# Performance work log

Hardware: AMD Instinct MI355X
Metric: run time of the kernel (lower is better)

## Reference

```python
import jax, jax.numpy as jnp
import numpy as np

EPS = 1e-6


def layernorm(x, w, b):
    m = jnp.mean(x, axis=-1, keepdims=True)
    v = jnp.var(x, axis=-1, keepdims=True)
    return (x - m) * jax.lax.rsqrt(v + EPS) * w + b


def rotate_half(x):
    x1, x2 = jnp.split(x, 2, axis=-1)
    return jnp.concatenate((-x2, x1), axis=-1)


def setup_inputs() -> dict:
    key = jax.random.key(0)
    ks = jax.random.split(key, 16)
    T, D, H, HD, I = 16384, 1280, 16, 80, 5120
    NSEG = 16
    inp = {
        "hidden_states": jax.random.normal(ks[0], (T, D), jnp.float32),
        "cos": jax.random.uniform(ks[1], (T, HD), jnp.float32),
        "sin": jax.random.uniform(ks[2], (T, HD), jnp.float32),
        "ln1_w": jnp.ones((D,), jnp.float32),
        "ln1_b": jnp.zeros((D,), jnp.float32),
        "ln2_w": jnp.ones((D,), jnp.float32),
        "ln2_b": jnp.zeros((D,), jnp.float32),
        "qkv_w": jax.random.normal(ks[3], (3 * D, D), jnp.float32) * 0.02,
        "qkv_b": jnp.zeros((3 * D,), jnp.float32),
        "proj_w": jax.random.normal(ks[4], (D, D), jnp.float32) * 0.02,
        "proj_b": jnp.zeros((D,), jnp.float32),
        "fc1_w": jax.random.normal(ks[5], (I, D), jnp.float32) * 0.02,
        "fc1_b": jnp.zeros((I,), jnp.float32),
        "fc2_w": jax.random.normal(ks[6], (D, I), jnp.float32) * 0.02,
        "fc2_b": jnp.zeros((D,), jnp.float32),
        "cu_seqlens": jnp.arange(NSEG + 1, dtype=jnp.int32) * (T // NSEG),
    }
    return inp


def reference(hidden_states, cos, sin, ln1_w, ln1_b, ln2_w, ln2_b,
              qkv_w, qkv_b, proj_w, proj_b, fc1_w, fc1_b, fc2_w, fc2_b,
              cu_seqlens):
    T, D = hidden_states.shape
    H = 16
    HD = D // H
    nseg = cu_seqlens.shape[0] - 1  # equal-length segments by construction
    L = T // nseg

    x = layernorm(hidden_states, ln1_w, ln1_b)
    qkv = (x @ qkv_w.T + qkv_b).reshape(T, 3, H, HD)
    q, k, v = qkv[:, 0], qkv[:, 1], qkv[:, 2]  # [T, H, HD]

    # RoPE in fp32, cos/sin broadcast over heads
    c = cos[:, None, :]
    s = sin[:, None, :]
    q = q * c + rotate_half(q) * s
    k = k * c + rotate_half(k) * s

    # block-diagonal varlen attention: reshape into [nseg, L, H, HD]
    qs = q.reshape(nseg, L, H, HD)
    ks = k.reshape(nseg, L, H, HD)
    vs = v.reshape(nseg, L, H, HD)
    scale = 1.0 / jnp.sqrt(jnp.asarray(HD, jnp.float32))
    scores = jnp.einsum('slhd,smhd->shlm', qs, ks) * scale
    probs = jax.nn.softmax(scores, axis=-1)
    attn = jnp.einsum('shlm,smhd->slhd', probs, vs).reshape(T, D)

    attn_out = attn @ proj_w.T + proj_b
    h = hidden_states + attn_out

    y = layernorm(h, ln2_w, ln2_b)
    mlp = (jax.nn.silu(y @ fc1_w.T + fc1_b)) @ fc2_w.T + fc2_b
    return h + mlp
```

## Files before the change

### kernel.cpp

```cpp
#include <hip/hip_runtime.h>
#include <hip/hip_bf16.h>
#include <hip/hip_fp16.h>

typedef _Float16 f16;
typedef _Float16 f16x2 __attribute__((ext_vector_type(2)));
typedef _Float16 f16x4 __attribute__((ext_vector_type(4)));
typedef _Float16 f16x8 __attribute__((ext_vector_type(8)));
typedef float f32x4 __attribute__((ext_vector_type(4)));
typedef float f32x16 __attribute__((ext_vector_type(16)));
typedef int i32x4 __attribute__((ext_vector_type(4)));

#define T_TOK 16384
#define D_MOD 1280
#define N_QKV 3840
#define I_MLP 5120
#define N_HEAD 16
#define HD 80
#define SEG_L 1024

__device__ __forceinline__ void async16(const void* g, void* l) {
    __builtin_amdgcn_global_load_lds(
        (const __attribute__((address_space(1))) void*)g,
        (__attribute__((address_space(3))) void*)l, 16, 0, 0);
}

#define BAR()        asm volatile("s_barrier" ::: "memory")
#define WAIT_LGKM0() do { asm volatile("s_waitcnt lgkmcnt(0)" ::: "memory"); \
                          __builtin_amdgcn_sched_barrier(0); } while (0)
#define WAIT_VM(n)   asm volatile("s_waitcnt vmcnt(" #n ")" ::: "memory")

__device__ __forceinline__ int f2i(f16x2 v) { int r; __builtin_memcpy(&r, &v, 4); return r; }
__device__ __forceinline__ f16x2 i2f(int v) { f16x2 r; __builtin_memcpy(&r, &v, 4); return r; }

__global__ __launch_bounds__(256) void cast_f32_f16(
    const float* __restrict__ src, f16* __restrict__ dst, int n) {
    int i = blockIdx.x * 256 + threadIdx.x;
    if (i < n) dst[i] = (f16)src[i];
}

template <typename TIN>
__global__ __launch_bounds__(256) void ln_kernel(
    const TIN* __restrict__ x, const float* __restrict__ w,
    const float* __restrict__ b, f16* __restrict__ out) {
    const int t = blockIdx.x;
    const TIN* row = x + (size_t)t * D_MOD;
    float vals[5];
    float s = 0.f, s2 = 0.f;
    for (int i = 0; i < 5; ++i) {
        float v = (float)row[threadIdx.x + i * 256];
        vals[i] = v; s += v; s2 += v * v;
    }
    for (int off = 32; off > 0; off >>= 1) {
        s  += __shfl_down(s, off);
        s2 += __shfl_down(s2, off);
    }
    __shared__ float rs[4], rs2[4];
    int wv = threadIdx.x >> 6;
    if ((threadIdx.x & 63) == 0) { rs[wv] = s; rs2[wv] = s2; }
    __syncthreads();
    s  = rs[0] + rs[1] + rs[2] + rs[3];
    s2 = rs2[0] + rs2[1] + rs2[2] + rs2[3];
    float m = s * (1.f / D_MOD);
    float var = s2 * (1.f / D_MOD) - m * m;
    float rstd = rsqrtf(var + 1e-6f);
    for (int i = 0; i < 5; ++i) {
        int c = threadIdx.x + i * 256;
        out[(size_t)t * D_MOD + c] = (f16)((vals[i] - m) * rstd * w[c] + b[c]);
    }
}

__global__ __launch_bounds__(256) void rope_inplace(
    f16* __restrict__ q, f16* __restrict__ k,
    const float* __restrict__ cosb, const float* __restrict__ sinb) {
    int i = blockIdx.x * 256 + threadIdx.x;
    if (i >= T_TOK * N_HEAD * 40) return;
    int d = i % 40;
    int th = i / 40;
    int h = th & 15;
    int t = th >> 4;
    size_t i0 = ((size_t)h * T_TOK + t) * HD + d;
    size_t i1 = i0 + 40;
    float c0 = cosb[t * HD + d],      s0 = sinb[t * HD + d];
    float c1 = cosb[t * HD + d + 40], s1 = sinb[t * HD + d + 40];
    {
        float x0 = (float)q[i0], x1 = (float)q[i1];
        q[i0] = (f16)(x0 * c0 - x1 * s0);
        q[i1] = (f16)(x1 * c1 + x0 * s1);
    }
    {
        float x0 = (float)k[i0], x1 = (float)k[i1];
        k[i0] = (f16)(x0 * c0 - x1 * s0);
        k[i1] = (f16)(x1 * c1 + x0 * s1);
    }
}

#define EPI_QKV   0
#define EPI_PROJ  1
#define EPI_SILU  2
#define EPI_FC2A  3
#define EPI_FC2B  4

#define READ_A(MH) \
    _Pragma("unroll") for (int mi = 0; mi < 4; ++mi) { \
        const f16* pa = &LB[lb][MH][(wr * 64 + mi * 16 + lane16) * 64]; \
        aF[mi][0] = *(const f16x8*)&pa[ch0]; \
        aF[mi][1] = *(const f16x8*)&pa[ch1]; \
    }
#define READ_B(NH) \
    _Pragma("unroll") for (int ni = 0; ni < 2; ++ni) { \
        const f16* pb = &LB[lb][2 + NH][(wc * 32 + ni * 16 + lane16) * 64]; \
        bF[ni][0] = *(const f16x8*)&pb[ch0]; \
        bF[ni][1] = *(const f16x8*)&pb[ch1]; \
    }
#define DO_MFMA(MH, NH) \
    __builtin_amdgcn_s_setprio(1); \
    _Pragma("unroll") for (int mi = 0; mi < 4; ++mi) \
    _Pragma("unroll") for (int ni = 0; ni < 2; ++ni) { \
        acc[MH][NH][mi][ni] = __builtin_amdgcn_mfma_f32_16x16x32_f16( \
            aF[mi][0], bF[ni][0], acc[MH][NH][mi][ni], 0, 0, 0); \
        acc[MH][NH][mi][ni] = __builtin_amdgcn_mfma_f32_16x16x32_f16( \
            aF[mi][1], bF[ni][1], acc[MH][NH][mi][ni], 0, 0, 0); \
    } \
    __builtin_amdgcn_s_setprio(0);

template <int EPI>
__global__ __launch_bounds__(512, 2) void gemm_bt(
    const f16* __restrict__ A, const f16* __restrict__ B,
    const float* __restrict__ bias, const void* __restrict__ resid,
    void* __restrict__ out0, f16* __restrict__ out1, f16* __restrict__ out2,
    int M, int N, int K, int lda, int ldb, int ldo) {
    __shared__ __align__(16) f16 LB[2][4][8192];
    const int tid = threadIdx.x;
    const int w = tid >> 6;
    const int l = tid & 63;
    const int lane16 = l & 15, quad = l >> 4;
    const int wr = w >> 2, wc = w & 3;

    const int nx = gridDim.x;
    int id = blockIdx.y * nx + blockIdx.x;
    const int nwg = nx * gridDim.y;
    int tile = ((nwg & 7) == 0) ? ((id & 7) * (nwg >> 3) + (id >> 3)) : id;
    const int m0 = (tile / nx) * 256;
    const int n0 = (tile % nx) * 256;
    const int NT = K >> 6;

    const int rr = tid >> 3;
    const int cc = (tid & 7) ^ (rr & 7);
    const size_t ga_off = (size_t)rr * lda + cc * 8;
    const size_t gb_off = (size_t)rr * ldb + cc * 8;
    const int lds_off = w * 512;
    const int swz = lane16 & 7;
    const int ch0 = ((0 * 4 + quad) ^ swz) * 8;
    const int ch1 = ((1 * 4 + quad) ^ swz) * 8;

    f32x4 acc[2][2][4][2];
#pragma unroll
    for (int a = 0; a < 2; ++a)
#pragma unroll
        for (int b2 = 0; b2 < 2; ++b2)
#pragma unroll
            for (int c = 0; c < 4; ++c)
#pragma unroll
                for (int d = 0; d < 2; ++d)
                    acc[a][b2][c][d] = (f32x4){0.f, 0.f, 0.f, 0.f};

    const f16* Abase = A + (size_t)m0 * lda;
    const f16* Bbase = B + (size_t)n0 * ldb;
    auto stageA = [&](int buf, int ph, int t) {
        const f16* g = Abase + (size_t)(ph * 128) * lda + (size_t)t * 64 + ga_off;
        f16* lr = &LB[buf][ph][0] + lds_off;
        async16(g, lr);
        async16(g + (size_t)64 * lda, lr + 4096);
    };
    auto stageB = [&](int buf, int ph, int t) {
        const f16* g = Bbase + (size_t)(ph * 128) * ldb + (size_t)t * 64 + gb_off;
        f16* lr = &LB[buf][2 + ph][0] + lds_off;
        async16(g, lr);
        async16(g + (size_t)64 * ldb, lr + 4096);
    };

    stageA(0, 0, 0); stageB(0, 1, 0); stageA(0, 1, 0); stageB(0, 0, 0);
    if (NT > 1) {
        stageA(1, 0, 1); stageB(1, 1, 1); stageA(1, 1, 1);
        WAIT_VM(6);
    } else {
        WAIT_VM(0);
    }
    BAR();

    for (int t = 0; t < NT; ++t) {
        const int lb = t & 1;
        f16x8 aF[4][2], bF[2][2];
        READ_A(0); READ_B(0);
        { int tau = t + 1; if (tau < NT) stageB(tau & 1, 0, tau); }
        BAR(); WAIT_LGKM0();
        DO_MFMA(0, 0);
        BAR();
        READ_B(1);
        { int tau = t + 2; if (tau < NT) stageA(tau & 1, 0, tau); }
        BAR(); WAIT_LGKM0();
        DO_MFMA(0, 1);
        BAR();
        READ_A(1);
        { int tau = t + 2; if (tau < NT) stageB(tau & 1, 1, tau); }
        BAR(); WAIT_LGKM0();
        DO_MFMA(1, 1);
        BAR();
        READ_B(0);
        { int tau = t + 2; if (tau < NT) stageA(tau & 1, 1, tau); }
        BAR(); WAIT_LGKM0();
        DO_MFMA(1, 0);
        if (t < NT - 2) { WAIT_VM(6); } else { WAIT_VM(0); }
        BAR();
    }

#pragma unroll
    for (int mh = 0; mh < 2; ++mh)
#pragma unroll
    for (int mi = 0; mi < 4; ++mi) {
        const int row = m0 + mh * 128 + wr * 64 + mi * 16 + quad * 4;
#pragma unroll
        for (int nh = 0; nh < 2; ++nh)
#pragma unroll
        for (int ni = 0; ni < 2; ++ni) {
            const int col = n0 + nh * 128 + wc * 32 + ni * 16 + lane16;
            const f32x4 v4 = acc[mh][nh][mi][ni];
            float bv = (EPI == EPI_FC2B) ? 0.f : bias[col];
            if (EPI == EPI_QKV) {
                int g = col / D_MOD;
                int rem = col - g * D_MOD;
                int h = rem / HD, d = rem - h * HD;
                if (g == 2) {
                    f16x4 pk;
#pragma unroll
                    for (int r2 = 0; r2 < 4; ++r2) pk[r2] = (f16)(v4[r2] + bv);
                    f16* dst = out2 + ((size_t)h * HD + d) * T_TOK + row;
                    *(f16x4*)dst = pk;
                } else {
                    f16* dst = (g == 0) ? (f16*)out0 : out1;
                    size_t base = ((size_t)h * T_TOK) * HD + d;
#pragma unroll
                    for (int r2 = 0; r2 < 4; ++r2) {
                        float v = v4[r2] + bv;
                        dst[base + (size_t)(row + r2) * HD] = (f16)v;
                    }
                }
            } else {
#pragma unroll
                for (int r2 = 0; r2 < 4; ++r2) {
                    float v = v4[r2] + bv;
                    size_t idx = (size_t)(row + r2) * ldo + col;
                    if (EPI == EPI_PROJ) {
                        ((f16*)out0)[idx] = (f16)(v + ((const float*)resid)[idx]);
                    } else if (EPI == EPI_SILU) {
                        ((f16*)out0)[idx] = (f16)(v / (1.f + __expf(-v)));
                    } else if (EPI == EPI_FC2A) {
                        ((float*)out0)[idx] = v + (float)((const f16*)resid)[idx];
                    } else {
                        ((float*)out0)[idx] += v;
                    }
                }
            }
        }
    }
}

#undef READ_A
#undef READ_B
#undef DO_MFMA

__global__ __launch_bounds__(256, 2) void attn_kernel(
    const f16* __restrict__ q, const f16* __restrict__ k,
    const f16* __restrict__ vt, f16* __restrict__ out) {
    const int bid0 = blockIdx.x;
    const int bid = (bid0 & 7) * 256 + (bid0 >> 3);
    const int s = bid >> 7, h = (bid >> 3) & 15, qt = bid & 7;
    const int t0 = s * SEG_L;
    const int tid = threadIdx.x;
    const int w = tid >> 6, l = tid & 63;
    const int l31 = l & 31, hi = l >> 5;

    __shared__ __align__(16) f16 lK[64 * 128];
    __shared__ __align__(16) f16 lVt[96 * 64];
    __shared__ float lInv[128];

    const f16 scale = (f16)0.16132167f;

    const int qrow_g = t0 + qt * 128 + w * 32 + l31;
    const f16* qp = q + ((size_t)h * T_TOK + qrow_g) * HD;
    f16x8 qf[5];
#pragma unroll
    for (int ks = 0; ks < 5; ++ks) {
        f16x8 v = *(const f16x8*)&qp[(ks * 2 + hi) * 8];
        qf[ks] = v * scale;
    }

    const f16* kbase  = k  + (size_t)h * T_TOK * HD + (size_t)t0 * HD;
    const f16* vtbase = vt + (size_t)h * HD * T_TOK + t0;

    if (tid < 128) {
        int r = 80 + (tid >> 3), c = tid & 7;
        *(f16x8*)&lVt[r * 64 + ((c ^ (r & 7)) * 8)] = (f16x8){0,0,0,0,0,0,0,0};
    }

    f16x8 kreg[3], vreg[3];
    auto ld_tile = [&](int kt) {
#pragma unroll
        for (int j = 0; j < 3; ++j) {
            int idx = tid + j * 256;
            if (idx < 640) {
                int r = idx / 10, c = idx - r * 10;
                kreg[j] = *(const f16x8*)&kbase[(size_t)(kt * 64 + r) * HD + c * 8];
                int rv = idx >> 3, cv = idx & 7;
                vreg[j] = *(const f16x8*)&vtbase[(size_t)rv * T_TOK + kt * 64 + cv * 8];
            }
        }
    };
    auto st_tile = [&]() {
#pragma unroll
        for (int j = 0; j < 3; ++j) {
            int idx = tid + j * 256;
            if (idx < 640) {
                int r = idx / 10, c = idx - r * 10;
                *(f16x8*)&lK[r * 128 + ((c ^ (r & 7)) * 8)] = kreg[j];
                int rv = idx >> 3, cv = idx & 7;
                *(f16x8*)&lVt[rv * 64 + ((cv ^ (rv & 7)) * 8)] = vreg[j];
            }
        }
    };

    float lrow = 0.f;
    f32x16 zz;
#pragma unroll
    for (int i = 0; i < 16; ++i) zz[i] = 0.f;
    f32x16 oacc[3];
    oacc[0] = zz; oacc[1] = zz; oacc[2] = zz;

    ld_tile(0);
    st_tile();
    __syncthreads();

    for (int kt = 0; kt < 16; ++kt) {
        if (kt < 15) ld_tile(kt + 1);

#pragma unroll
        for (int ct = 0; ct < 2; ++ct) {
            f32x16 sc = zz;
#pragma unroll
            for (int ks = 0; ks < 5; ++ks) {
                const int row = ct * 32 + l31;
                f16x8 kf = *(const f16x8*)&lK[row * 128 +
                              (((ks * 2 + hi) ^ (l31 & 7)) * 8)];
                sc = __builtin_amdgcn_mfma_f32_32x32x16_f16(kf, qf[ks], sc, 0, 0, 0);
            }
            float pf[16];
#pragma unroll
            for (int r = 0; r < 16; ++r) {
                float p = __builtin_exp2f(fminf(sc[r], 14.f));
                lrow += p;
                pf[r] = p;
            }
            f16x2 own[4][2];
            int prt[4][2];
#pragma unroll
            for (int d = 0; d < 4; ++d) {
                own[d][0] = (f16x2){(f16)pf[4 * d + 0], (f16)pf[4 * d + 1]};
                own[d][1] = (f16x2){(f16)pf[4 * d + 2], (f16)pf[4 * d + 3]};
                prt[d][0] = __shfl_xor(f2i(own[d][0]), 32);
                prt[d][1] = __shfl_xor(f2i(own[d][1]), 32);
            }
#pragma unroll
            for (int kk2 = 0; kk2 < 2; ++kk2) {
                const int De = 2 * kk2, Do = 2 * kk2 + 1;
                i32x4 av;
                av[0] = hi ? prt[Do][0] : f2i(own[De][0]);
                av[1] = hi ? prt[Do][1] : f2i(own[De][1]);
                av[2] = hi ? f2i(own[Do][0]) : prt[De][0];
                av[3] = hi ? f2i(own[Do][1]) : prt[De][1];
                f16x8 af;
                __builtin_memcpy(&af, &av, 16);
                const int kkg = ct * 2 + kk2;
#pragma unroll
                for (int nt = 0; nt < 3; ++nt) {
                    const int vrow = nt * 32 + l31;
                    f16x8 vf = *(const f16x8*)&lVt[vrow * 64 +
                                  (((kkg * 2 + hi) ^ (l31 & 7)) * 8)];
                    oacc[nt] = __builtin_amdgcn_mfma_f32_32x32x16_f16(
                        af, vf, oacc[nt], 0, 0, 0);
                }
            }
        }
        __syncthreads();
        if (kt < 15) st_tile();
        __syncthreads();
    }

    lrow += __shfl_xor(lrow, 32);
    float inv = 1.f / lrow;
    lInv[w * 32 + l31] = inv;

    f16* obase = out + (size_t)(t0 + qt * 128 + w * 32) * D_MOD + h * HD;
#pragma unroll
    for (int nt = 0; nt < 3; ++nt) {
        const int hd = nt * 32 + l31;
        if (nt < 2 || l31 < 16) {
#pragma unroll
            for (int r = 0; r < 16; ++r) {
                const int qrow = (r & 3) + 8 * (r >> 2) + 4 * hi;
                obase[(size_t)qrow * D_MOD + hd] =
                    (f16)(oacc[nt][r] * lInv[w * 32 + qrow]);
            }
        }
    }
}

extern "C" void kernel_launch(void* const* d_in, const int* in_sizes, int n_in,
                              void* d_out, int out_size, void* d_ws, size_t ws_size,
                              hipStream_t stream) {
    const float* hidden = (const float*)d_in[0];
    const float* cosb   = (const float*)d_in[1];
    const float* sinb   = (const float*)d_in[2];
    const float* ln1w   = (const float*)d_in[3];
    const float* ln1b   = (const float*)d_in[4];
    const float* ln2w   = (const float*)d_in[5];
    const float* ln2b   = (const float*)d_in[6];
    const float* qkvw   = (const float*)d_in[7];
    const float* qkvb   = (const float*)d_in[8];
    const float* projw  = (const float*)d_in[9];
    const float* projb  = (const float*)d_in[10];
    const float* fc1w   = (const float*)d_in[11];
    const float* fc1b   = (const float*)d_in[12];
    const float* fc2w   = (const float*)d_in[13];
    const float* fc2b   = (const float*)d_in[14];
    float* out = (float*)d_out;

    f16* wqkv  = (f16*)d_ws;
    f16* wproj = wqkv  + 4915200;
    f16* wfc1  = wproj + 1638400;
    f16* wfc2  = wfc1  + 6553600;
    f16* qf    = wfc2  + 6553600;
    f16* kf    = qf    + 20971520;
    f16* vf    = kf    + 20971520;
    f16* xf    = vf    + 20971520;
    f16* hbuf  = xf    + 20971520;
    f16* attnf  = xf;
    f16* yf     = qf;
    f16* fc1out = kf;

    cast_f32_f16<<<(4915200 + 255) / 256, 256, 0, stream>>>(qkvw, wqkv, 4915200);
    cast_f32_f16<<<(1638400 + 255) / 256, 256, 0, stream>>>(projw, wproj, 1638400);
    cast_f32_f16<<<(6553600 + 255) / 256, 256, 0, stream>>>(fc1w, wfc1, 6553600);
    cast_f32_f16<<<(6553600 + 255) / 256, 256, 0, stream>>>(fc2w, wfc2, 6553600);

    ln_kernel<float><<<T_TOK, 256, 0, stream>>>(hidden, ln1w, ln1b, xf);

    gemm_bt<EPI_QKV><<<dim3(N_QKV / 256, T_TOK / 256), 512, 0, stream>>>(
        xf, wqkv, qkvb, nullptr, qf, kf, vf,
        T_TOK, N_QKV, D_MOD, D_MOD, D_MOD, 0);

    rope_inplace<<<(T_TOK * N_HEAD * 40) / 256, 256, 0, stream>>>(qf, kf, cosb, sinb);

    attn_kernel<<<2048, 256, 0, stream>>>(qf, kf, vf, attnf);

    gemm_bt<EPI_PROJ><<<dim3(D_MOD / 256, T_TOK / 256), 512, 0, stream>>>(
        attnf, wproj, projb, hidden, hbuf, nullptr, nullptr,
        T_TOK, D_MOD, D_MOD, D_MOD, D_MOD, D_MOD);

    ln_kernel<f16><<<T_TOK, 256, 0, stream>>>(hbuf, ln2w, ln2b, yf);

    for (int c = 0; c < 2; ++c) {
        gemm_bt<EPI_SILU><<<dim3(2560 / 256, T_TOK / 256), 512, 0, stream>>>(
            yf, wfc1 + (size_t)c * 2560 * D_MOD, fc1b + c * 2560, nullptr,
            fc1out, nullptr, nullptr,
            T_TOK, 2560, D_MOD, D_MOD, D_MOD, 2560);
        if (c == 0) {
            gemm_bt<EPI_FC2A><<<dim3(D_MOD / 256, T_TOK / 256), 512, 0, stream>>>(
                fc1out, wfc2, fc2b, hbuf, out, nullptr, nullptr,
                T_TOK, D_MOD, 2560, 2560, I_MLP, D_MOD);
        } else {
            gemm_bt<EPI_FC2B><<<dim3(D_MOD / 256, T_TOK / 256), 512, 0, stream>>>(
                fc1out, wfc2 + 2560, fc2b, nullptr, out, nullptr, nullptr,
                T_TOK, D_MOD, 2560, 2560, I_MLP, D_MOD);
        }
    }
}
```

Before: 1.393 ms.

## Restructure GEMM main loop with register double-buffered fragments and overlapped LDS reads

The GEMM inner loop is rescheduled so LDS fragment reads for the next phase are issued before the current phase's MFMAs, using two register sets for A and B fragments. Each phase now needs one barrier plus LDS wait instead of two barriers. The prologue loads both stages up front, and the A fragments for the next tile are prefetched at the end of each iteration. The aim is to hide LDS latency behind MFMA work and cut synchronization, at the cost of more VGPRs, which could hurt occupancy or cause spills under launch_bounds(512,2).

```diff
diff --git a/kernel.cpp b/kernel.cpp
--- a/kernel.cpp
+++ b/kernel.cpp
@@ -28,9 +28,9 @@
 #define WAIT_LGKM0() do { asm volatile("s_waitcnt lgkmcnt(0)" ::: "memory"); \
                           __builtin_amdgcn_sched_barrier(0); } while (0)
 #define WAIT_VM(n)   asm volatile("s_waitcnt vmcnt(" #n ")" ::: "memory")
+#define SCHED0()     __builtin_amdgcn_sched_barrier(0)
 
 __device__ __forceinline__ int f2i(f16x2 v) { int r; __builtin_memcpy(&r, &v, 4); return r; }
-__device__ __forceinline__ f16x2 i2f(int v) { f16x2 r; __builtin_memcpy(&r, &v, 4); return r; }
 
 __global__ __launch_bounds__(256) void cast_f32_f16(
     const float* __restrict__ src, f16* __restrict__ dst, int n) {
@@ -100,27 +100,25 @@
 #define EPI_FC2A  3
 #define EPI_FC2B  4
 
-#define READ_A(MH) \
+#define RD_A(DST, MH, BUF) \
     _Pragma("unroll") for (int mi = 0; mi < 4; ++mi) { \
-        const f16* pa = &LB[lb][MH][(wr * 64 + mi * 16 + lane16) * 64]; \
-        aF[mi][0] = *(const f16x8*)&pa[ch0]; \
-        aF[mi][1] = *(const f16x8*)&pa[ch1]; \
-    }
-#define READ_B(NH) \
+        const f16* pa = &LB[BUF][MH][(wr * 64 + mi * 16 + lane16) * 64]; \
+        DST[mi][0] = *(const f16x8*)&pa[ch0]; \
+        DST[mi][1] = *(const f16x8*)&pa[ch1]; \
+    }
+#define RD_B(DST, NH, BUF) \
     _Pragma("unroll") for (int ni = 0; ni < 2; ++ni) { \
-        const f16* pb = &LB[lb][2 + NH][(wc * 32 + ni * 16 + lane16) * 64]; \
-        bF[ni][0] = *(const f16x8*)&pb[ch0]; \
-        bF[ni][1] = *(const f16x8*)&pb[ch1]; \
-    }
-#define DO_MFMA(MH, NH) \
+        const f16* pb = &LB[BUF][2 + NH][(wc * 32 + ni * 16 + lane16) * 64]; \
+        DST[ni][0] = *(const f16x8*)&pb[ch0]; \
+        DST[ni][1] = *(const f16x8*)&pb[ch1]; \
+    }
+#define MFMA_PH(MH, NH, AARR, BARR) \
     __builtin_amdgcn_s_setprio(1); \
+    _Pragma("unroll") for (int h2 = 0; h2 < 2; ++h2) \
     _Pragma("unroll") for (int mi = 0; mi < 4; ++mi) \
-    _Pragma("unroll") for (int ni = 0; ni < 2; ++ni) { \
+    _Pragma("unroll") for (int ni = 0; ni < 2; ++ni) \
         acc[MH][NH][mi][ni] = __builtin_amdgcn_mfma_f32_16x16x32_f16( \
-            aF[mi][0], bF[ni][0], acc[MH][NH][mi][ni], 0, 0, 0); \
-        acc[MH][NH][mi][ni] = __builtin_amdgcn_mfma_f32_16x16x32_f16( \
-            aF[mi][1], bF[ni][1], acc[MH][NH][mi][ni], 0, 0, 0); \
-    } \
+            AARR[mi][h2], BARR[ni][h2], acc[MH][NH][mi][ni], 0, 0, 0); \
     __builtin_amdgcn_s_setprio(0);
 
 template <int EPI>
@@ -179,39 +177,39 @@
         async16(g + (size_t)64 * ldb, lr + 4096);
     };
 
-    stageA(0, 0, 0); stageB(0, 1, 0); stageA(0, 1, 0); stageB(0, 0, 0);
-    if (NT > 1) {
-        stageA(1, 0, 1); stageB(1, 1, 1); stageA(1, 1, 1);
-        WAIT_VM(6);
-    } else {
-        WAIT_VM(0);
-    }
+    f16x8 aF0[4][2], aF1[4][2], bF0[2][2], bF1[2][2];
+
+    stageA(0, 0, 0); stageB(0, 0, 0); stageB(0, 1, 0); stageA(0, 1, 0);
+    if (NT > 1) { stageA(1, 0, 1); stageB(1, 0, 1); stageB(1, 1, 1); stageA(1, 1, 1); }
+    WAIT_VM(0);
+    BAR();
+    RD_A(aF0, 0, 0);
+    WAIT_LGKM0();
     BAR();
 
     for (int t = 0; t < NT; ++t) {
         const int lb = t & 1;
-        f16x8 aF[4][2], bF[2][2];
-        READ_A(0); READ_B(0);
-        { int tau = t + 1; if (tau < NT) stageB(tau & 1, 0, tau); }
-        BAR(); WAIT_LGKM0();
-        DO_MFMA(0, 0);
-        BAR();
-        READ_B(1);
-        { int tau = t + 2; if (tau < NT) stageA(tau & 1, 0, tau); }
-        BAR(); WAIT_LGKM0();
-        DO_MFMA(0, 1);
-        BAR();
-        READ_A(1);
-        { int tau = t + 2; if (tau < NT) stageB(tau & 1, 1, tau); }
-        BAR(); WAIT_LGKM0();
-        DO_MFMA(1, 1);
-        BAR();
-        READ_B(0);
-        { int tau = t + 2; if (tau < NT) stageA(tau & 1, 1, tau); }
-        BAR(); WAIT_LGKM0();
-        DO_MFMA(1, 0);
+        RD_B(bF0, 0, lb);
+        RD_B(bF1, 1, lb);
+        if (t + 2 < NT) stageA(lb, 0, t + 2);
+        SCHED0();
+        MFMA_PH(0, 0, aF0, bF0);
+        WAIT_LGKM0(); BAR();
+        RD_A(aF1, 1, lb);
+        if (t + 2 < NT) stageB(lb, 1, t + 2);
+        SCHED0();
+        MFMA_PH(0, 1, aF0, bF1);
+        WAIT_LGKM0(); BAR();
+        if (t + 2 < NT) stageA(lb, 1, t + 2);
         if (t < NT - 2) { WAIT_VM(6); } else { WAIT_VM(0); }
-        BAR();
+        SCHED0();
+        MFMA_PH(1, 1, aF1, bF1);
+        WAIT_LGKM0(); BAR();
+        if (t + 2 < NT) stageB(lb, 0, t + 2);
+        if (t + 1 < NT) RD_A(aF0, 0, lb ^ 1);
+        SCHED0();
+        MFMA_PH(1, 0, aF1, bF0);
+        WAIT_LGKM0(); BAR();
     }
 
 #pragma unroll
@@ -265,9 +263,9 @@
     }
 }
 
-#undef READ_A
-#undef READ_B
-#undef DO_MFMA
+#undef RD_A
+#undef RD_B
+#undef MFMA_PH
 
 __global__ __launch_bounds__(256, 2) void attn_kernel(
     const f16* __restrict__ q, const f16* __restrict__ k,
```

Result: no change. 1.405 ms (+0.9%).
